# Performance work log

Measured on AMD Instinct MI355X. Metric: run time of the kernel, lower is better.

The kernel has to match this reference:

```python
import jax, jax.numpy as jnp
import numpy as np

B, C_IN, H, W = 2, 32, 512, 512
HIDDEN, SIZE = 768, 16
LATENT, NUM_CLASS = 128, 21
HP, WP = H // SIZE, W // SIZE
EPS = 1e-8
TEMP = 0.5


def setup_inputs() -> dict:
    key = jax.random.key(0)
    k1, k2, k3, k4, k5 = jax.random.split(key, 5)
    x = jax.random.normal(k1, (B, C_IN, H, W), dtype=jnp.float32)
    mask = jax.random.randint(k2, (B, NUM_CLASS, HP, WP), 0, 2).astype(jnp.int32)
    conv_w = jax.random.normal(k3, (HIDDEN, C_IN, SIZE, SIZE), dtype=jnp.float32) * 0.02
    conv_b = jax.random.normal(k4, (HIDDEN,), dtype=jnp.float32) * 0.02
    latent = jax.random.normal(k5, (1, LATENT * NUM_CLASS, HIDDEN), dtype=jnp.float32)
    return {"x": x, "mask": mask, "conv_w": conv_w, "conv_b": conv_b, "latent": latent}


def reference(x, mask, conv_w, conv_b, latent):
    # Patch embedding: Conv2d(kernel=stride=16) -> (B, HIDDEN, HP, WP)
    patch = jax.lax.conv_general_dilated(
        x, conv_w, window_strides=(SIZE, SIZE), padding='VALID',
        dimension_numbers=('NCHW', 'OIHW', 'NCHW'))
    patch = patch + conv_b[None, :, None, None]
    Bv = x.shape[0]
    N = HP * WP
    patch = patch.reshape(Bv, HIDDEN, N).transpose(0, 2, 1)  # (B, N, D)
    lat = jnp.broadcast_to(latent, (Bv, LATENT * NUM_CLASS, HIDDEN))  # (B, LC, D)

    # Cosine similarity as normalized batched matmul (same math as
    # torch CosineSimilarity over broadcast (B, LC, N, D))
    dots = jnp.einsum('bld,bnd->bln', lat, patch)  # (B, LC, N)
    lat_norm = jnp.linalg.norm(lat, axis=-1)       # (B, LC)
    pat_norm = jnp.linalg.norm(patch, axis=-1)     # (B, N)
    sim = dots / jnp.maximum(lat_norm[:, :, None] * pat_norm[:, None, :], EPS)

    sim = sim.reshape(Bv, LATENT, NUM_CLASS, HP, WP).mean(axis=1)  # (B, C, HP, WP)

    m = mask.astype(jnp.float32) >= 0.5
    s = jnp.sum(jnp.where(m, jnp.exp(sim / TEMP), 0.0))
    return -jnp.log(s)
```

## Files before the change

kernel.cpp:

```cpp
#include <hip/hip_runtime.h>
#include <math.h>

#define B_     2
#define CIN    32
#define HH     512
#define WW     512
#define HID    768
#define SZ     16
#define NPATCH 1024
#define KDIM   8192
#define NCLS   21
#define LAT    128
#define LC     2688
#define NP     (B_ * NPATCH)

#define NB_CL  63
#define NB_W4  1536
#define NB_XT  2048

typedef __attribute__((ext_vector_type(8))) short short8;
typedef __attribute__((ext_vector_type(4))) float f32x4;

__device__ __forceinline__ ushort f2bf(float f) {
    union { float f; unsigned u; } v; v.f = f;
    unsigned r = (v.u + 0x7fff + ((v.u >> 16) & 1)) >> 16;
    return (ushort)r;
}
__device__ __forceinline__ float bf2f(ushort u) {
    union { unsigned u; float f; } v; v.u = (unsigned)u << 16;
    return v.f;
}

__device__ __forceinline__ void gload16(const void* g, void* l) {
    __builtin_amdgcn_global_load_lds(
        (const __attribute__((address_space(1))) unsigned int*)g,
        (__attribute__((address_space(3))) unsigned int*)l, 16, 0, 0);
}

__global__ __launch_bounds__(256) void k_scale(const float* __restrict__ lat,
                                               float* __restrict__ scale) {
    int wid  = blockIdx.x * 4 + (threadIdx.x >> 6);
    int lane = threadIdx.x & 63;
    const float* row = lat + (size_t)wid * HID;
    float s = 0.f;
#pragma unroll
    for (int q = 0; q < HID / 64; ++q) {
        float v = row[lane + q * 64];
        s += v * v;
    }
#pragma unroll
    for (int off = 32; off >= 1; off >>= 1) s += __shfl_xor(s, off, 64);
    if (lane == 0) scale[wid] = 1.0f / (128.0f * sqrtf(s));
}

__global__ __launch_bounds__(256) void k_prep(const float* __restrict__ w,
                                              const float* __restrict__ x,
                                              const float* __restrict__ lat,
                                              const float* __restrict__ scale,
                                              ushort* __restrict__ wb,
                                              ushort* __restrict__ xb,
                                              float* __restrict__ classlat) {
    const int bid = blockIdx.x;
    const int t   = threadIdx.x;

    if (bid < NB_CL) {
        const int cls  = bid / 3;
        const int dseg = bid % 3;
        __shared__ float sc_sh[LAT];
        if (t < LAT) sc_sh[t] = scale[t * NCLS + cls];
        __syncthreads();

        const float* src = lat + (size_t)cls * HID + dseg * 256 + t;
        float a = 0.f;
        for (int u0 = 0; u0 < LAT; u0 += 8) {
            float v[8];
#pragma unroll
            for (int q = 0; q < 8; ++q)
                v[q] = src[(size_t)(u0 + q) * (NCLS * HID)];
#pragma unroll
            for (int q = 0; q < 8; ++q) a += v[q] * sc_sh[u0 + q];
        }
        classlat[cls * HID + dseg * 256 + t] = a;
    } else if (bid < NB_CL + NB_W4) {
        const int cb = bid - NB_CL;
        float4 vv[4];
#pragma unroll
        for (int k = 0; k < 4; ++k)
            vv[k] = *(const float4*)(w + ((size_t)cb * 1024 + k * 256 + t) * 4);
#pragma unroll
        for (int k = 0; k < 4; ++k) {
            ushort4 o;
            o.x = f2bf(vv[k].x); o.y = f2bf(vv[k].y);
            o.z = f2bf(vv[k].z); o.w = f2bf(vv[k].w);
            *(ushort4*)(wb + ((size_t)cb * 1024 + k * 256 + t) * 4) = o;
        }
    } else {
        __shared__ ushort sh[32 * 264];
        const int cvb = bid - (NB_CL + NB_W4);
        const int b  = cvb >> 10;
        const int c  = (cvb >> 5) & 31;
        const int ph = cvb & 31;
        const float* src = x + (((size_t)(b * CIN + c) * HH) + (size_t)ph * 16) * WW;

        float4 vv[8];
#pragma unroll
        for (int q = 0; q < 8; ++q) {
            int f  = q * 256 + t;
            int i  = f >> 7;
            int w4 = f & 127;
            vv[q] = *(const float4*)(src + (size_t)i * WW + w4 * 4);
        }
#pragma unroll
        for (int q = 0; q < 8; ++q) {
            int f  = q * 256 + t;
            int i  = f >> 7;
            int w4 = f & 127;
            int pw = w4 >> 2, j0 = (w4 & 3) * 4;
            ushort4 o;
            o.x = f2bf(vv[q].x); o.y = f2bf(vv[q].y);
            o.z = f2bf(vv[q].z); o.w = f2bf(vv[q].w);
            *(ushort4*)&sh[pw * 264 + i * 16 + j0] = o;
        }
        __syncthreads();

        ushort* dst = xb + ((size_t)(b * 1024 + ph * 32) << 13) + c * 256;
        short8 rv[4];
#pragma unroll
        for (int q = 0; q < 4; ++q) {
            int s  = q * 256 + t;
            int pw = s >> 5;
            int o8 = (s & 31) * 8;
            rv[q] = *(const short8*)&sh[pw * 264 + o8];
        }
#pragma unroll
        for (int q = 0; q < 4; ++q) {
            int s  = q * 256 + t;
            int pw = s >> 5;
            int o8 = (s & 31) * 8;
            *(short8*)&dst[((size_t)pw << 13) + o8] = rv[q];
        }
    }
}

template <int SPLITK>
__global__ __launch_bounds__(256) void k_gemm(const ushort* __restrict__ xb,
                                              const ushort* __restrict__ wb,
                                              ushort* __restrict__ pbuf) {
    constexpr int KS = KDIM / SPLITK;
    __shared__ ushort Als[128 * 64];
    __shared__ ushort Bls[128 * 64];

    const int flat = blockIdx.x + 16 * (blockIdx.y + 6 * blockIdx.z);
    constexpr int nwg = 96 * SPLITK;
    const int wg = (flat & 7) * (nwg >> 3) + (flat >> 3);
    const int bz = wg / 96;
    const int rr = wg - bz * 96;
    const int by = rr % 6;
    const int bx = rr / 6;

    const int tid  = threadIdx.x;
    const int wv   = tid >> 6;
    const int lane = tid & 63;
    const int wm   = (wv >> 1) * 64;
    const int wn   = (wv & 1) * 64;

    const size_t abase = ((size_t)bx * 128) * KDIM + (size_t)bz * KS;
    const size_t bbase = ((size_t)by * 128) * KDIM + (size_t)bz * KS;

    const int srow  = wv * 8 + (lane >> 3);
    const int skoff = (((lane & 7) ^ (lane >> 3)) * 8);

    f32x4 acc[4][4];
#pragma unroll
    for (int m = 0; m < 4; ++m)
#pragma unroll
        for (int n = 0; n < 4; ++n) acc[m][n] = (f32x4)(0.f);

    const int fr = lane & 15, fq = lane >> 4;
    const int frx = (fr & 7) * 8;

    for (int kk = 0; kk < KS; kk += 64) {
#pragma unroll
        for (int q = 0; q < 4; ++q) {
            const int row = q * 32 + srow;
            gload16(&xb[abase + (size_t)row * KDIM + kk + skoff], &Als[q * 2048 + wv * 512]);
            gload16(&wb[bbase + (size_t)row * KDIM + kk + skoff], &Bls[q * 2048 + wv * 512]);
        }
        __syncthreads();

#pragma unroll
        for (int s = 0; s < 2; ++s) {
            short8 af[4], bf[4];
#pragma unroll
            for (int m = 0; m < 4; ++m)
                af[m] = *(const short8*)&Als[(wm + m * 16 + fr) * 64 + ((s * 32 + fq * 8) ^ frx)];
#pragma unroll
            for (int n = 0; n < 4; ++n)
                bf[n] = *(const short8*)&Bls[(wn + n * 16 + fr) * 64 + ((s * 32 + fq * 8) ^ frx)];
#pragma unroll
            for (int m = 0; m < 4; ++m)
#pragma unroll
                for (int n = 0; n < 4; ++n)
                    acc[m][n] = __builtin_amdgcn_mfma_f32_16x16x32_bf16(af[m], bf[n], acc[m][n], 0, 0, 0);
        }
        __syncthreads();
    }

#pragma unroll
    for (int m = 0; m < 4; ++m) {
#pragma unroll
        for (int n = 0; n < 4; ++n) {
            int col = by * 128 + wn + n * 16 + fr;
#pragma unroll
            for (int j = 0; j < 4; ++j) {
                int row = bx * 128 + wm + m * 16 + fq * 4 + j;
                pbuf[((size_t)row * SPLITK + bz) * HID + col] = f2bf(acc[m][n][j]);
            }
        }
    }
}

template <int SPLITK>
__global__ __launch_bounds__(256) void k_final(const ushort* __restrict__ pbuf,
                                               const float* __restrict__ conv_b,
                                               const float* __restrict__ classlat,
                                               const int* __restrict__ mask,
                                               float* __restrict__ partial) {
    const int p = blockIdx.x;
    const int b = p >> 10, n = p & 1023;
    const int t = threadIdx.x;
    const int lane = t & 63, wv = t >> 6;

    __shared__ ushort sh[SPLITK * HID];
    const ushort* pb = pbuf + (size_t)p * (SPLITK * HID);
    for (int i = t; i < SPLITK * HID / 8; i += 256)
        *(short8*)&sh[i * 8] = *(const short8*)&pb[(size_t)i * 8];
    __syncthreads();

    float f0 = conv_b[t], f1 = conv_b[t + 256], f2 = conv_b[t + 512];
#pragma unroll
    for (int z = 0; z < SPLITK; ++z) {
        f0 += bf2f(sh[z * HID + t]);
        f1 += bf2f(sh[z * HID + t + 256]);
        f2 += bf2f(sh[z * HID + t + 512]);
    }

    __shared__ float wsum[4];
    __shared__ float wdot[4][NCLS];
    __shared__ float cpart[NCLS];

    float ss = f0 * f0 + f1 * f1 + f2 * f2;
#pragma unroll
    for (int off = 32; off >= 1; off >>= 1) ss += __shfl_xor(ss, off, 64);
    if (lane == 0) wsum[wv] = ss;

    float dots[NCLS];
#pragma unroll
    for (int c = 0; c < NCLS; ++c) {
        const float* cl = classlat + c * HID;
        dots[c] = cl[t] * f0 + cl[t + 256] * f1 + cl[t + 512] * f2;
    }
#pragma unroll
    for (int c = 0; c < NCLS; ++c) {
        float v = dots[c];
#pragma unroll
        for (int off = 32; off >= 1; off >>= 1) v += __shfl_xor(v, off, 64);
        if (lane == 0) wdot[wv][c] = v;
    }
    __syncthreads();

    if (t < NCLS) {
        float tot  = wsum[0] + wsum[1] + wsum[2] + wsum[3];
        float invn = 1.0f / sqrtf(tot);
        float dot  = wdot[0][t] + wdot[1][t] + wdot[2][t] + wdot[3][t];
        float sim  = dot * invn;
        int   mv   = mask[(size_t)(b * NCLS + t) * NPATCH + n];
        cpart[t]   = (mv != 0) ? expf(sim * 2.0f) : 0.0f;
    }
    __syncthreads();
    if (t == 0) {
        float s = 0.f;
#pragma unroll
        for (int c = 0; c < NCLS; ++c) s += cpart[c];
        partial[p] = s;
    }
}

__global__ __launch_bounds__(256) void k_reduce(const float* __restrict__ partial,
                                                float* __restrict__ out) {
    int t = threadIdx.x;
    float s = 0.f;
    for (int i = t; i < NP; i += 256) s += partial[i];
#pragma unroll
    for (int off = 32; off >= 1; off >>= 1) s += __shfl_xor(s, off, 64);
    __shared__ float ws[4];
    if ((t & 63) == 0) ws[t >> 6] = s;
    __syncthreads();
    if (t == 0) out[0] = -logf(ws[0] + ws[1] + ws[2] + ws[3]);
}

extern "C" void kernel_launch(void* const* d_in, const int* in_sizes, int n_in,
                              void* d_out, int out_size, void* d_ws, size_t ws_size,
                              hipStream_t stream) {
    const float* x      = (const float*)d_in[0];
    const int*   mask   = (const int*)d_in[1];
    const float* conv_w = (const float*)d_in[2];
    const float* conv_b = (const float*)d_in[3];
    const float* latent = (const float*)d_in[4];
    float* out = (float*)d_out;

    const size_t xb_bytes   = (size_t)NP * KDIM * 2;
    const size_t wb_bytes   = (size_t)HID * KDIM * 2;
    const size_t pslice     = (size_t)NP * HID * 2;
    const size_t small_need = (size_t)NCLS * HID * 4 + NP * 4 + LC * 4 + 256;

    char* base = (char*)d_ws;
    ushort* xb   = (ushort*)base;
    ushort* wb   = (ushort*)(base + xb_bytes);
    ushort* pbuf = (ushort*)(base + xb_bytes + wb_bytes);

    int splitk = 1;
    const size_t fixed = xb_bytes + wb_bytes + small_need;
    if (ws_size >= fixed + 8 * pslice)      splitk = 8;
    else if (ws_size >= fixed + 4 * pslice) splitk = 4;
    else if (ws_size >= fixed + 2 * pslice) splitk = 2;

    float* classlat = (float*)(base + xb_bytes + wb_bytes + (size_t)splitk * pslice);
    float* partial  = classlat + NCLS * HID;
    float* scale    = partial + NP;

    k_scale<<<LC / 4, 256, 0, stream>>>(latent, scale);
    k_prep<<<NB_CL + NB_W4 + NB_XT, 256, 0, stream>>>(conv_w, x, latent, scale,
                                                      wb, xb, classlat);

    dim3 g(NP / 128, HID / 128, splitk);
    switch (splitk) {
        case 8: k_gemm<8><<<g, 256, 0, stream>>>(xb, wb, pbuf); break;
        case 4: k_gemm<4><<<g, 256, 0, stream>>>(xb, wb, pbuf); break;
        case 2: k_gemm<2><<<g, 256, 0, stream>>>(xb, wb, pbuf); break;
        default: k_gemm<1><<<g, 256, 0, stream>>>(xb, wb, pbuf); break;
    }

    switch (splitk) {
        case 8: k_final<8><<<NP, 256, 0, stream>>>(pbuf, conv_b, classlat, mask, partial); break;
        case 4: k_final<4><<<NP, 256, 0, stream>>>(pbuf, conv_b, classlat, mask, partial); break;
        case 2: k_final<2><<<NP, 256, 0, stream>>>(pbuf, conv_b, classlat, mask, partial); break;
        default: k_final<1><<<NP, 256, 0, stream>>>(pbuf, conv_b, classlat, mask, partial); break;
    }
    k_reduce<<<1, 256, 0, stream>>>(partial, out);
}
```

Measured before the change: 85.25 us.

## Enlarge GEMM tile to 256x128 with 512 threads and fold latent-norm kernel into prep

The GEMM block tile grows from 128x128 to 256x128 and runs with 512 threads (8 waves), so each B tile loaded into LDS is reused across twice as many rows and total global traffic for W drops. The grid halves accordingly. Separately, the k_scale kernel is removed and the per-latent inverse norms are computed inside the class-latent blocks of k_prep, saving one launch and a scratch buffer. Risks: the doubled LDS footprint and 512-thread blocks reduce occupancy and grid size (fewer workgroups for 256 CUs at low split-k), and the 63 class blocks now each recompute 128 row norms, making that prep path heavier.

```diff
diff --git a/kernel.cpp b/kernel.cpp
--- a/kernel.cpp
+++ b/kernel.cpp
@@ -37,26 +37,9 @@
         (__attribute__((address_space(3))) unsigned int*)l, 16, 0, 0);
 }
 
-__global__ __launch_bounds__(256) void k_scale(const float* __restrict__ lat,
-                                               float* __restrict__ scale) {
-    int wid  = blockIdx.x * 4 + (threadIdx.x >> 6);
-    int lane = threadIdx.x & 63;
-    const float* row = lat + (size_t)wid * HID;
-    float s = 0.f;
-#pragma unroll
-    for (int q = 0; q < HID / 64; ++q) {
-        float v = row[lane + q * 64];
-        s += v * v;
-    }
-#pragma unroll
-    for (int off = 32; off >= 1; off >>= 1) s += __shfl_xor(s, off, 64);
-    if (lane == 0) scale[wid] = 1.0f / (128.0f * sqrtf(s));
-}
-
 __global__ __launch_bounds__(256) void k_prep(const float* __restrict__ w,
                                               const float* __restrict__ x,
                                               const float* __restrict__ lat,
-                                              const float* __restrict__ scale,
                                               ushort* __restrict__ wb,
                                               ushort* __restrict__ xb,
                                               float* __restrict__ classlat) {
@@ -66,8 +49,29 @@
     if (bid < NB_CL) {
         const int cls  = bid / 3;
         const int dseg = bid % 3;
+        const int lane = t & 63, wvv = t >> 6;
         __shared__ float sc_sh[LAT];
-        if (t < LAT) sc_sh[t] = scale[t * NCLS + cls];
+
+        for (int q = 0; q < 32; q += 2) {
+            int u0 = wvv * 32 + q;
+            const float* r0 = lat + (size_t)(u0 * NCLS + cls) * HID;
+            const float* r1 = lat + (size_t)((u0 + 1) * NCLS + cls) * HID;
+            float s0 = 0.f, s1 = 0.f;
+#pragma unroll
+            for (int e = 0; e < HID / 64; ++e) {
+                float a = r0[lane + e * 64]; s0 += a * a;
+                float b2 = r1[lane + e * 64]; s1 += b2 * b2;
+            }
+#pragma unroll
+            for (int off = 32; off >= 1; off >>= 1) {
+                s0 += __shfl_xor(s0, off, 64);
+                s1 += __shfl_xor(s1, off, 64);
+            }
+            if (lane == 0) {
+                sc_sh[u0]     = 1.0f / (128.0f * sqrtf(s0));
+                sc_sh[u0 + 1] = 1.0f / (128.0f * sqrtf(s1));
+            }
+        }
         __syncthreads();
 
         const float* src = lat + (size_t)cls * HID + dseg * 256 + t;
@@ -143,18 +147,18 @@
 }
 
 template <int SPLITK>
-__global__ __launch_bounds__(256) void k_gemm(const ushort* __restrict__ xb,
+__global__ __launch_bounds__(512) void k_gemm(const ushort* __restrict__ xb,
                                               const ushort* __restrict__ wb,
                                               ushort* __restrict__ pbuf) {
     constexpr int KS = KDIM / SPLITK;
-    __shared__ ushort Als[128 * 64];
+    __shared__ ushort Als[256 * 64];
     __shared__ ushort Bls[128 * 64];
 
-    const int flat = blockIdx.x + 16 * (blockIdx.y + 6 * blockIdx.z);
-    constexpr int nwg = 96 * SPLITK;
+    const int flat = blockIdx.x + 8 * (blockIdx.y + 6 * blockIdx.z);
+    constexpr int nwg = 48 * SPLITK;
     const int wg = (flat & 7) * (nwg >> 3) + (flat >> 3);
-    const int bz = wg / 96;
-    const int rr = wg - bz * 96;
+    const int bz = wg / 48;
+    const int rr = wg - bz * 48;
     const int by = rr % 6;
     const int bx = rr / 6;
 
@@ -164,7 +168,7 @@
     const int wm   = (wv >> 1) * 64;
     const int wn   = (wv & 1) * 64;
 
-    const size_t abase = ((size_t)bx * 128) * KDIM + (size_t)bz * KS;
+    const size_t abase = ((size_t)bx * 256) * KDIM + (size_t)bz * KS;
     const size_t bbase = ((size_t)by * 128) * KDIM + (size_t)bz * KS;
 
     const int srow  = wv * 8 + (lane >> 3);
@@ -182,9 +186,15 @@
     for (int kk = 0; kk < KS; kk += 64) {
 #pragma unroll
         for (int q = 0; q < 4; ++q) {
-            const int row = q * 32 + srow;
-            gload16(&xb[abase + (size_t)row * KDIM + kk + skoff], &Als[q * 2048 + wv * 512]);
-            gload16(&wb[bbase + (size_t)row * KDIM + kk + skoff], &Bls[q * 2048 + wv * 512]);
+            const int row = q * 64 + srow;
+            gload16(&xb[abase + (size_t)row * KDIM + kk + skoff],
+                    &Als[(q * 64 + wv * 8) * 64]);
+        }
+#pragma unroll
+        for (int q = 0; q < 2; ++q) {
+            const int row = q * 64 + srow;
+            gload16(&wb[bbase + (size_t)row * KDIM + kk + skoff],
+                    &Bls[(q * 64 + wv * 8) * 64]);
         }
         __syncthreads();
 
@@ -213,7 +223,7 @@
             int col = by * 128 + wn + n * 16 + fr;
 #pragma unroll
             for (int j = 0; j < 4; ++j) {
-                int row = bx * 128 + wm + m * 16 + fq * 4 + j;
+                int row = bx * 256 + wm + m * 16 + fq * 4 + j;
                 pbuf[((size_t)row * SPLITK + bz) * HID + col] = f2bf(acc[m][n][j]);
             }
         }
@@ -312,7 +322,7 @@
     const size_t xb_bytes   = (size_t)NP * KDIM * 2;
     const size_t wb_bytes   = (size_t)HID * KDIM * 2;
     const size_t pslice     = (size_t)NP * HID * 2;
-    const size_t small_need = (size_t)NCLS * HID * 4 + NP * 4 + LC * 4 + 256;
+    const size_t small_need = (size_t)NCLS * HID * 4 + NP * 4 + 256;
 
     char* base = (char*)d_ws;
     ushort* xb   = (ushort*)base;
@@ -327,18 +337,16 @@
 
     float* classlat = (float*)(base + xb_bytes + wb_bytes + (size_t)splitk * pslice);
     float* partial  = classlat + NCLS * HID;
-    float* scale    = partial + NP;
-
-    k_scale<<<LC / 4, 256, 0, stream>>>(latent, scale);
-    k_prep<<<NB_CL + NB_W4 + NB_XT, 256, 0, stream>>>(conv_w, x, latent, scale,
+
+    k_prep<<<NB_CL + NB_W4 + NB_XT, 256, 0, stream>>>(conv_w, x, latent,
                                                       wb, xb, classlat);
 
-    dim3 g(NP / 128, HID / 128, splitk);
+    dim3 g(NP / 256, HID / 128, splitk);
     switch (splitk) {
-        case 8: k_gemm<8><<<g, 256, 0, stream>>>(xb, wb, pbuf); break;
-        case 4: k_gemm<4><<<g, 256, 0, stream>>>(xb, wb, pbuf); break;
-        case 2: k_gemm<2><<<g, 256, 0, stream>>>(xb, wb, pbuf); break;
-        default: k_gemm<1><<<g, 256, 0, stream>>>(xb, wb, pbuf); break;
+        case 8: k_gemm<8><<<g, 512, 0, stream>>>(xb, wb, pbuf); break;
+        case 4: k_gemm<4><<<g, 512, 0, stream>>>(xb, wb, pbuf); break;
+        case 2: k_gemm<2><<<g, 512, 0, stream>>>(xb, wb, pbuf); break;
+        default: k_gemm<1><<<g, 512, 0, stream>>>(xb, wb, pbuf); break;
     }
 
     switch (splitk) {
```

After: 85.77 us. No clear change (+0.6%).
